# Kernel tuning notes

Measured on AMD Instinct MI355X. Metric: run time of the kernel, lower is better.

## Reference

```python
import jax, jax.numpy as jnp
import numpy as np

MAX_RADIUS = 1.5
NUM_BASIS = 10
CS, CV = 16, 4              # scalar / vector multiplicities (input = query = key = output irreps)
DIM = CS + 3 * CV           # 28
SILU_GAIN = 1.679           # e3nn normalize2mom gain for silu


def _sus(x):
    # e3nn soft_unit_step: exp(-1/x) for x>0 else 0
    xp = jnp.where(x > 0, x, 1.0)
    return jnp.where(x > 0, jnp.exp(-1.0 / xp), 0.0)


def _fc(emb, w1, w2):
    # FullyConnectedNet([NUM_BASIS, 16, numel], act=silu), fan-in normalized
    h = SILU_GAIN * jax.nn.silu(emb @ w1 / jnp.sqrt(float(NUM_BASIS)))
    return h @ w2 / jnp.sqrt(16.0)


def _tp(fs, fv, sh1, w):
    # FullyConnectedTensorProduct((CS x0e + CV x1o) x (1x0e + 1x1o)) with per-edge weights w [...,400]
    # paths: 0e*0e->0e, 0e*1o->1o, 1o*0e->1o, 1o*1o->0e (sh l=0 component == 1)
    i0 = CS * CS; i1 = i0 + CS * CV; i2 = i1 + CV * CV
    lead = w.shape[:-1]
    w1 = w[..., :i0].reshape(lead + (CS, CS))
    w2 = w[..., i0:i1].reshape(lead + (CS, CV))
    w3 = w[..., i1:i2].reshape(lead + (CV, CV))
    w4 = w[..., i2:].reshape(lead + (CV, CS))
    out_s = (jnp.einsum('...c,...co->...o', fs, w1) / jnp.sqrt(float(CS))
             + jnp.einsum('...cx,...x,...co->...o', fv, sh1, w4) / jnp.sqrt(3.0 * CV)) / jnp.sqrt(2.0)
    out_v = (jnp.einsum('...c,...x,...co->...ox', fs, sh1, w2) / jnp.sqrt(float(CS))
             + jnp.einsum('...cx,...co->...ox', fv, w3) / jnp.sqrt(float(CV))) / jnp.sqrt(2.0)
    return out_s, out_v


def _forward(f, pos, wq_s, wq_v, fck_w1, fck_w2, fcv_w1, fcv_w2, dot_ws, dot_wv):
    B, N, _ = f.shape
    fs = f[..., :CS]                                    # [B,N,CS]
    fv = f[..., CS:].reshape(B, N, CV, 3)               # [B,N,CV,3]
    valid = jnp.any(f != 0, axis=-1)                    # mask of non-padded nodes

    # dense radius graph: i = dst, j = src; edge_vec = pos[src] - pos[dst]
    dvec = pos[:, None, :, :] - pos[:, :, None, :]      # [B,i,j,3]
    dist = jnp.sqrt(jnp.sum(dvec * dvec, axis=-1) + 1e-12)
    eye = jnp.eye(N, dtype=bool)
    mask = (dist < MAX_RADIUS) & (~eye)[None] & valid[:, :, None] & valid[:, None, :]
    sh1 = jnp.sqrt(3.0) * dvec / dist[..., None]        # component-normalized l=1 spherical harmonics

    # soft_one_hot_linspace, basis='smooth_finite', cutoff=True, scaled by sqrt(NB)
    step = MAX_RADIUS / (NUM_BASIS + 1)
    centers = jnp.linspace(0.0, MAX_RADIUS, NUM_BASIS + 2)[1:-1]
    diff = (dist[..., None] - centers) / step
    emb = (1.14136 * np.e ** 2) * _sus(diff + 1.0) * _sus(1.0 - diff)
    emb = emb * jnp.sqrt(float(NUM_BASIS))
    cutoff = _sus(10.0 * (1.0 - dist / MAX_RADIUS)) * mask

    # q = h_q(f): per-l linear
    q_s = fs @ wq_s / jnp.sqrt(float(CS))
    q_v = jnp.einsum('bncx,co->bnox', fv, wq_v) / jnp.sqrt(float(CV))

    wk = _fc(emb, fck_w1, fck_w2)                       # [B,N,N,400] per-edge TP weights
    wv = _fc(emb, fcv_w1, fcv_w2)
    k_s, k_v = _tp(fs[:, None], fv[:, None], sh1, wk)   # gather f[src] via broadcast over dst axis
    v_s, v_v = _tp(fs[:, None], fv[:, None], sh1, wv)

    # dot(q[dst], k) -> scalar per edge
    score = (jnp.einsum('bic,bijd,cd->bij', q_s, k_s, dot_ws) / jnp.sqrt(float(CS))
             + jnp.einsum('bicx,bijdx,cd->bij', q_v, k_v, dot_wv) / jnp.sqrt(3.0 * CV)) / jnp.sqrt(2.0)
    log_exp = cutoff * score
    z = jnp.sum(log_exp, axis=-1)                       # scatter-sum over src per dst node
    z = jnp.where(z == 0, 1.0, z)
    alpha = log_exp / z[:, :, None]
    r = jax.nn.relu(alpha)
    att = jnp.where(r > 0, jnp.sqrt(jnp.where(r > 0, r, 1.0)), 0.0)

    out_s = jnp.einsum('bij,bijo->bio', att, v_s)       # scatter-aggregate
    out_v = jnp.einsum('bij,bijox->biox', att, v_v)
    out = jnp.concatenate([out_s, out_v.reshape(B, N, 3 * CV)], axis=-1)
    return out * valid[..., None].astype(out.dtype)


def setup_inputs() -> dict:
    key = jax.random.key(0)
    ks = jax.random.split(key, 10)
    B, N = 4, 192
    NUMEL = CS * CS + CS * CV + CV * CV + CV * CS       # 400
    n = jax.random.normal
    return {
        'f': n(ks[0], (B, N, DIM), dtype=jnp.float32),
        'pos': 5.0 * jax.random.uniform(ks[1], (B, N, 3), dtype=jnp.float32),
        'wq_s': n(ks[2], (CS, CS), dtype=jnp.float32),
        'wq_v': n(ks[3], (CV, CV), dtype=jnp.float32),
        'fck_w1': n(ks[4], (NUM_BASIS, 16), dtype=jnp.float32),
        'fck_w2': n(ks[5], (16, NUMEL), dtype=jnp.float32),
        'fcv_w1': n(ks[6], (NUM_BASIS, 16), dtype=jnp.float32),
        'fcv_w2': n(ks[7], (16, NUMEL), dtype=jnp.float32),
        'dot_ws': n(ks[8], (CS, CS), dtype=jnp.float32),
        'dot_wv': n(ks[9], (CV, CV), dtype=jnp.float32),
    }


def reference(f, pos, wq_s, wq_v, fck_w1, fck_w2, fcv_w1, fcv_w2, dot_ws, dot_wv):
    return _forward(f, pos, wq_s, wq_v, fck_w1, fck_w2, fcv_w1, fcv_w2, dot_ws, dot_wv)
```

## Files before the change

### kernel.cpp

```cpp
#include <hip/hip_runtime.h>
#include <math.h>


#define NN 192
#define TSTRIDE 2560
#define MAXM 192
#define NPB 3

constexpr float C1   = 0.17677669529663687f;
constexpr float C2   = 0.17677669529663687f;
constexpr float C3   = 0.35355339059327373f;
constexpr float C4   = 0.20412414523193154f;
constexpr float CS1f = 0.17677669529663687f;
constexpr float CS2f = 0.20412414523193154f;
constexpr float RS10 = 0.31622776601683794f;
constexpr float GAIN4 = 1.679f * 0.25f;
constexpr float SQRT3 = 1.7320508075688772f;
constexpr float CEMB = (float)(1.14136 * 7.3890560989306495 * 3.1622776601683795);

__global__ __launch_bounds__(256) void precomp(
  const float* __restrict__ f, const float* __restrict__ wq_s, const float* __restrict__ wq_v,
  const float* __restrict__ w2k, const float* __restrict__ w2v,
  const float* __restrict__ dws, const float* __restrict__ dwv,
  float* __restrict__ T, float* __restrict__ qd, float* __restrict__ validf, int BN)
{
  const int node0 = blockIdx.x * NPB;
  const int tid   = threadIdx.x;
  __shared__ float Wsh[12800];
  __shared__ float fsh[NPB][28];
  __shared__ float qs_sh[NPB][16], qv_sh[NPB][12];
  __shared__ int vsh[NPB];
  if (tid < NPB) vsh[tid] = 0;
  if (tid < NPB*28) {
    const int n = tid / 28, c = tid - n*28;
    fsh[n][c] = (node0 + n < BN) ? f[(node0 + n)*28 + c] : 0.f;
  }
  {
    float4* d = (float4*)Wsh;
    const float4* s0 = (const float4*)w2k;
    const float4* s1 = (const float4*)w2v;
    for (int q = tid; q < 1600; q += 256) { d[q] = s0[q]; d[1600 + q] = s1[q]; }
  }
  __syncthreads();
  if (tid < NPB*28) {
    const int n = tid / 28, c = tid - n*28;
    if (fsh[n][c] != 0.f) vsh[n] = 1;
    if (c < 16) {
      float a = 0.f;
      #pragma unroll
      for (int c2 = 0; c2 < 16; ++c2) a = fmaf(fsh[n][c2], wq_s[c2*16 + c], a);
      qs_sh[n][c] = a * 0.25f;
    } else {
      const int idx = c - 16, o = idx / 3, x = idx - o*3;
      float a = 0.f;
      #pragma unroll
      for (int c2 = 0; c2 < 4; ++c2) a = fmaf(fsh[n][16 + c2*3 + x], wq_v[c2*4 + o], a);
      qv_sh[n][idx] = a * 0.5f;
    }
  }
  __syncthreads();
  if (tid < NPB*28) {
    const int n = tid / 28, c = tid - n*28, node = node0 + n;
    if (node < BN) {
      if (c < 16) {
        float a = 0.f;
        #pragma unroll
        for (int c2 = 0; c2 < 16; ++c2) a = fmaf(qs_sh[n][c2], dws[c2*16 + c], a);
        qd[node*28 + c] = a * CS1f;
      } else {
        const int idx = c - 16, d2 = idx / 3, x = idx - d2*3;
        float a = 0.f;
        #pragma unroll
        for (int c2 = 0; c2 < 4; ++c2) a = fmaf(qv_sh[n][c2*3 + x], dwv[c2*4 + d2], a);
        qd[node*28 + c] = a * CS2f;
      }
      if (c == 0) validf[node] = vsh[n] ? 1.f : 0.f;
    }
  }

  for (int e = tid; e < NPB*2560; e += 256) {
    const int n = e / 2560;
    if (node0 + n >= BN) break;
    const int rr = e - n*2560;
    const int fc = rr >= 1280 ? 1 : 0;
    const int r = rr - fc*1280;
    const int h = r / 80, q = r - h*80;
    const float* W = Wsh + fc*6400 + h*400;
    const float* fn = fsh[n];
    float val = 0.f;
    if (q < 16) {
      #pragma unroll
      for (int c = 0; c < 16; ++c) val = fmaf(fn[c], W[c*16 + q], val);
      val *= C1;
    } else if (q < 20) {
      const int o = q - 16;
      #pragma unroll
      for (int c = 0; c < 16; ++c) val = fmaf(fn[c], W[256 + c*4 + o], val);
      val *= C2;
    } else if (q < 32) {
      const int p = q - 20, o = p / 3, x = p - o*3;
      #pragma unroll
      for (int c = 0; c < 4; ++c) val = fmaf(fn[16 + c*3 + x], W[320 + c*4 + o], val);
      val *= C3;
    } else {
      const int p = q - 32, o = p / 3, x = p - o*3;
      #pragma unroll
      for (int c = 0; c < 4; ++c) val = fmaf(fn[16 + c*3 + x], W[336 + c*16 + o], val);
      val *= C4;
    }
    T[(size_t)(node0 + n)*TSTRIDE + fc*1280 + (q >> 2)*64 + h*4 + (q & 3)] = val;
  }
}

__global__ __launch_bounds__(256) void se3_main(
  const float* __restrict__ pos, const float* __restrict__ w1k, const float* __restrict__ w1v,
  const float* __restrict__ T, const float* __restrict__ qd, const float* __restrict__ validf,
  float* __restrict__ out)
{
  const int bi = blockIdx.x;
  const int b = bi / NN, i = bi - b*NN;
  const int tid = threadIdx.x;
  const int lane = tid & 63, wid = tid >> 6;

  __shared__ float qd_sh[28];
  __shared__ float w1_sh[320];
  __shared__ int   s_node[MAXM];
  __shared__ float s_cut[MAXM], s_dist[MAXM];
  __shared__ float s_shx[MAXM], s_shy[MAXM], s_shz[MAXM];
  __shared__ float emb_sh[MAXM*10];
  __shared__ float Hk_sh[MAXM*16];
  __shared__ float Hv_sh[MAXM*16];
  __shared__ float le_sh[MAXM];
  __shared__ float att_sh[MAXM];
  __shared__ int   cnt_sh;
  __shared__ float red_sh[4];
  __shared__ float opart[4][28];

  if (tid < 28) qd_sh[tid] = qd[bi*28 + tid];
  if (tid < 160) {
    w1_sh[tid]       = w1k[tid] * RS10;
    w1_sh[160 + tid] = w1v[tid] * RS10;
  }
  if (tid == 0) cnt_sh = 0;
  const float pix = pos[bi*3+0], piy = pos[bi*3+1], piz = pos[bi*3+2];
  const float vali = validf[bi];
  __syncthreads();

  if (tid < NN) {
    const int nj = b*NN + tid;
    const float dx = pos[nj*3+0]-pix, dy = pos[nj*3+1]-piy, dz = pos[nj*3+2]-piz;
    const float dist = sqrtf(fmaf(dx,dx,fmaf(dy,dy,dz*dz)) + 1e-12f);
    if (tid != i && dist < 1.5f && vali != 0.f && validf[nj] != 0.f) {
      const float cut = expf(-1.f / (10.f * (1.f - dist * (1.f/1.5f))));
      if (cut > 0.f) {
        const int s = atomicAdd(&cnt_sh, 1);
        const float sc = SQRT3 / dist;
        s_node[s] = nj; s_cut[s] = cut; s_dist[s] = dist;
        s_shx[s] = dx*sc; s_shy[s] = dy*sc; s_shz[s] = dz*sc;
      }
    }
  }
  __syncthreads();
  const int M = cnt_sh;
  const int MK = M * 16;

  for (int idx = tid; idx < M*10; idx += 256) {
    const int pr = idx / 10, k = idx - pr*10;
    const float dd = (s_dist[pr] - (float)(k+1)*(1.5f/11.f)) * (11.f/1.5f);
    float e = 0.f;
    if (dd > -1.f && dd < 1.f) e = CEMB * expf(-1.f/(1.f+dd) - 1.f/(1.f-dd));
    emb_sh[idx] = e;
  }
  __syncthreads();

  for (int idx = tid; idx < M*32; idx += 256) {
    const int pr = idx >> 5, t = idx & 31, h = t & 15;
    const float* w = w1_sh + (t >> 4)*160;
    const float* e = emb_sh + pr*10;
    float s = 0.f;
    #pragma unroll
    for (int q = 0; q < 10; ++q) s = fmaf(e[q], w[q*16 + h], s);
    const float hh = GAIN4 * s / (1.f + expf(-s));
    float* dst = (t < 16) ? Hk_sh : Hv_sh;
    dst[pr*16 + h] = hh;
  }
  __syncthreads();

  for (int idx = tid; idx < MK; idx += 256) {
    const int pr = idx >> 4, h = idx & 15;
    const int node = s_node[pr];
    const float sx = s_shx[pr], sy = s_shy[pr], sz = s_shz[pr];
    const float a = Hk_sh[idx];
    const float4* b4 = (const float4*)(T + (size_t)node*TSTRIDE);
    float cc[80];
    float4* c4 = (float4*)cc;
    #pragma unroll
    for (int q = 0; q < 20; ++q) c4[q] = b4[q*16 + h];
    float s = 0.f;
    #pragma unroll
    for (int o = 0; o < 16; ++o) {
      const float t4 = fmaf(cc[32+3*o], sx, fmaf(cc[33+3*o], sy, cc[34+3*o]*sz));
      s = fmaf(qd_sh[o], cc[o] + t4, s);
    }
    #pragma unroll
    for (int o = 0; o < 4; ++o) {
      const float qvs = fmaf(qd_sh[16+3*o], sx, fmaf(qd_sh[17+3*o], sy, qd_sh[18+3*o]*sz));
      s = fmaf(qvs, cc[16+o], s);
      s = fmaf(qd_sh[16+3*o], cc[20+3*o+0], s);
      s = fmaf(qd_sh[17+3*o], cc[20+3*o+1], s);
      s = fmaf(qd_sh[18+3*o], cc[20+3*o+2], s);
    }
    s *= a;
    #pragma unroll
    for (int d = 1; d < 16; d <<= 1) s += __shfl_xor(s, d);
    if ((tid & 15) == 0) le_sh[pr] = s;
  }
  __syncthreads();

  float les = 0.f;
  if (tid < M) les = s_cut[tid] * le_sh[tid];
  float z = les;
  #pragma unroll
  for (int d = 1; d < 64; d <<= 1) z += __shfl_xor(z, d);
  if (lane == 0) red_sh[wid] = z;
  __syncthreads();
  z = red_sh[0] + red_sh[1] + red_sh[2] + red_sh[3];
  if (z == 0.f) z = 1.f;
  if (tid < M) {
    const float alpha = les / z;
    att_sh[tid] = alpha > 0.f ? sqrtf(alpha) : 0.f;
  }
  __syncthreads();

  float acc[28];
  #pragma unroll
  for (int c = 0; c < 28; ++c) acc[c] = 0.f;
  for (int idx = tid; idx < MK; idx += 256) {
    const int pr = idx >> 4, h = idx & 15;
    const int node = s_node[pr];
    const float sx = s_shx[pr], sy = s_shy[pr], sz = s_shz[pr];
    const float a = Hv_sh[idx] * att_sh[pr];
    const float4* b4 = (const float4*)(T + (size_t)node*TSTRIDE + 1280);
    float cc[80];
    float4* c4 = (float4*)cc;
    #pragma unroll
    for (int q = 0; q < 20; ++q) c4[q] = b4[q*16 + h];
    #pragma unroll
    for (int o = 0; o < 16; ++o) {
      const float t4 = fmaf(cc[32+3*o], sx, fmaf(cc[33+3*o], sy, cc[34+3*o]*sz));
      acc[o] = fmaf(a, cc[o] + t4, acc[o]);
    }
    const float ax = a*sx, ay = a*sy, az = a*sz;
    #pragma unroll
    for (int o = 0; o < 4; ++o) {
      const float t2 = cc[16+o];
      acc[16+3*o+0] = fmaf(ax, t2, fmaf(a, cc[20+3*o+0], acc[16+3*o+0]));
      acc[16+3*o+1] = fmaf(ay, t2, fmaf(a, cc[20+3*o+1], acc[16+3*o+1]));
      acc[16+3*o+2] = fmaf(az, t2, fmaf(a, cc[20+3*o+2], acc[16+3*o+2]));
    }
  }

  #pragma unroll
  for (int c = 0; c < 28; ++c) {
    float w = acc[c];
    #pragma unroll
    for (int d = 1; d < 64; d <<= 1) w += __shfl_xor(w, d);
    if (lane == 0) opart[wid][c] = w;
  }
  __syncthreads();
  if (tid < 28) out[bi*28 + tid] = opart[0][tid] + opart[1][tid] + opart[2][tid] + opart[3][tid];
}

extern "C" void kernel_launch(void* const* d_in, const int* in_sizes, int n_in,
                              void* d_out, int out_size, void* d_ws, size_t ws_size,
                              hipStream_t stream) {
  const float* f      = (const float*)d_in[0];
  const float* pos    = (const float*)d_in[1];
  const float* wq_s   = (const float*)d_in[2];
  const float* wq_v   = (const float*)d_in[3];
  const float* fck_w1 = (const float*)d_in[4];
  const float* fck_w2 = (const float*)d_in[5];
  const float* fcv_w1 = (const float*)d_in[6];
  const float* fcv_w2 = (const float*)d_in[7];
  const float* dot_ws = (const float*)d_in[8];
  const float* dot_wv = (const float*)d_in[9];
  float* outp = (float*)d_out;

  const int BN = in_sizes[0] / 28;

  float* T   = (float*)d_ws;
  float* qdp = T + (size_t)BN * TSTRIDE;
  float* vf  = qdp + (size_t)BN * 28;

  const int pblocks = (BN + NPB - 1) / NPB;
  precomp<<<pblocks, 256, 0, stream>>>(f, wq_s, wq_v, fck_w2, fcv_w2, dot_ws, dot_wv, T, qdp, vf, BN);
  se3_main<<<BN, 256, 0, stream>>>(pos, fck_w1, fcv_w1, T, qdp, vf, outp);
}
```

Baseline: 112.6 us.

## Repartition precompute kernel by weight row and node group

The precompute kernel now gives each block 16 nodes and one of 32 (fc,h) weight rows, loading only a 400-float weight row instead of staging the full 12800-float weight matrix in shared memory for 3 nodes. This removes the large per-block shared-memory fill and the low occupancy it forces. The query/dot and valid-flag work moves to the ch==0 blocks. The kernel drops its bounds checks and assumes BN is a multiple of 16. It also calls __syncthreads inside a branch, which is only safe because ch is uniform across the block.

Measured after the change: 105.0 us. 1.07x faster.

```diff
diff --git a/kernel.cpp b/kernel.cpp
--- a/kernel.cpp
+++ b/kernel.cpp
@@ -5,7 +5,7 @@
 #define NN 192
 #define TSTRIDE 2560
 #define MAXM 192
-#define NPB 3
+#define GN 16
 
 constexpr float C1   = 0.17677669529663687f;
 constexpr float C2   = 0.17677669529663687f;
@@ -18,50 +18,80 @@
 constexpr float SQRT3 = 1.7320508075688772f;
 constexpr float CEMB = (float)(1.14136 * 7.3890560989306495 * 3.1622776601683795);
 
-__global__ __launch_bounds__(256) void precomp(
+__global__ __launch_bounds__(256) void precomp_T(
   const float* __restrict__ f, const float* __restrict__ wq_s, const float* __restrict__ wq_v,
   const float* __restrict__ w2k, const float* __restrict__ w2v,
   const float* __restrict__ dws, const float* __restrict__ dwv,
-  float* __restrict__ T, float* __restrict__ qd, float* __restrict__ validf, int BN)
+  float* __restrict__ T, float* __restrict__ qd, float* __restrict__ validf)
 {
-  const int node0 = blockIdx.x * NPB;
-  const int tid   = threadIdx.x;
-  __shared__ float Wsh[12800];
-  __shared__ float fsh[NPB][28];
-  __shared__ float qs_sh[NPB][16], qv_sh[NPB][12];
-  __shared__ int vsh[NPB];
-  if (tid < NPB) vsh[tid] = 0;
-  if (tid < NPB*28) {
-    const int n = tid / 28, c = tid - n*28;
-    fsh[n][c] = (node0 + n < BN) ? f[(node0 + n)*28 + c] : 0.f;
-  }
+  const int bid = blockIdx.x;
+  const int ng = bid >> 5, ch = bid & 31;
+  const int fc = ch >> 4, h = ch & 15;
+  const int node0 = ng * GN;
+  const int tid = threadIdx.x;
+
+  __shared__ float Wrow[400];
+  __shared__ float fsh[GN][28];
+  __shared__ float qs_sh[GN][16], qv_sh[GN][12];
+  __shared__ int   vsh[GN];
+
   {
-    float4* d = (float4*)Wsh;
-    const float4* s0 = (const float4*)w2k;
-    const float4* s1 = (const float4*)w2v;
-    for (int q = tid; q < 1600; q += 256) { d[q] = s0[q]; d[1600 + q] = s1[q]; }
-  }
-  __syncthreads();
-  if (tid < NPB*28) {
-    const int n = tid / 28, c = tid - n*28;
-    if (fsh[n][c] != 0.f) vsh[n] = 1;
-    if (c < 16) {
-      float a = 0.f;
-      #pragma unroll
-      for (int c2 = 0; c2 < 16; ++c2) a = fmaf(fsh[n][c2], wq_s[c2*16 + c], a);
-      qs_sh[n][c] = a * 0.25f;
+    const float* Wsrc = (fc ? w2v : w2k) + h*400;
+    if (tid < 100) ((float4*)Wrow)[tid] = ((const float4*)Wsrc)[tid];
+    else if (tid < 212) ((float4*)fsh)[tid - 100] = ((const float4*)(f + node0*28))[tid - 100];
+    if (tid < GN) vsh[tid] = 0;
+  }
+  __syncthreads();
+
+  #pragma unroll
+  for (int k = 0; k < 5; ++k) {
+    const int out = tid + k*256;
+    const int n = out / 80, q = out - n*80;
+    const float* fn = fsh[n];
+    float val = 0.f;
+    if (q < 16) {
+      #pragma unroll
+      for (int c = 0; c < 16; ++c) val = fmaf(fn[c], Wrow[c*16 + q], val);
+      val *= C1;
+    } else if (q < 20) {
+      const int o = q - 16;
+      #pragma unroll
+      for (int c = 0; c < 16; ++c) val = fmaf(fn[c], Wrow[256 + c*4 + o], val);
+      val *= C2;
+    } else if (q < 32) {
+      const int p = q - 20, o = p / 3, x = p - o*3;
+      #pragma unroll
+      for (int c = 0; c < 4; ++c) val = fmaf(fn[16 + c*3 + x], Wrow[320 + c*4 + o], val);
+      val *= C3;
     } else {
-      const int idx = c - 16, o = idx / 3, x = idx - o*3;
-      float a = 0.f;
-      #pragma unroll
-      for (int c2 = 0; c2 < 4; ++c2) a = fmaf(fsh[n][16 + c2*3 + x], wq_v[c2*4 + o], a);
-      qv_sh[n][idx] = a * 0.5f;
-    }
-  }
-  __syncthreads();
-  if (tid < NPB*28) {
-    const int n = tid / 28, c = tid - n*28, node = node0 + n;
-    if (node < BN) {
+      const int p = q - 32, o = p / 3, x = p - o*3;
+      #pragma unroll
+      for (int c = 0; c < 4; ++c) val = fmaf(fn[16 + c*3 + x], Wrow[336 + c*16 + o], val);
+      val *= C4;
+    }
+    T[(size_t)(node0 + n)*TSTRIDE + fc*1280 + (q >> 2)*64 + h*4 + (q & 3)] = val;
+  }
+
+  if (ch == 0) {
+    for (int t = tid; t < GN*28; t += 256) {
+      const int n = t / 28, c = t - n*28;
+      if (fsh[n][c] != 0.f) vsh[n] = 1;
+      if (c < 16) {
+        float a = 0.f;
+        #pragma unroll
+        for (int c2 = 0; c2 < 16; ++c2) a = fmaf(fsh[n][c2], wq_s[c2*16 + c], a);
+        qs_sh[n][c] = a * 0.25f;
+      } else {
+        const int idx = c - 16, o = idx / 3, x = idx - o*3;
+        float a = 0.f;
+        #pragma unroll
+        for (int c2 = 0; c2 < 4; ++c2) a = fmaf(fsh[n][16 + c2*3 + x], wq_v[c2*4 + o], a);
+        qv_sh[n][idx] = a * 0.5f;
+      }
+    }
+    __syncthreads();
+    for (int t = tid; t < GN*28; t += 256) {
+      const int n = t / 28, c = t - n*28, node = node0 + n;
       if (c < 16) {
         float a = 0.f;
         #pragma unroll
@@ -76,39 +106,6 @@
       }
       if (c == 0) validf[node] = vsh[n] ? 1.f : 0.f;
     }
-  }
-
-  for (int e = tid; e < NPB*2560; e += 256) {
-    const int n = e / 2560;
-    if (node0 + n >= BN) break;
-    const int rr = e - n*2560;
-    const int fc = rr >= 1280 ? 1 : 0;
-    const int r = rr - fc*1280;
-    const int h = r / 80, q = r - h*80;
-    const float* W = Wsh + fc*6400 + h*400;
-    const float* fn = fsh[n];
-    float val = 0.f;
-    if (q < 16) {
-      #pragma unroll
-      for (int c = 0; c < 16; ++c) val = fmaf(fn[c], W[c*16 + q], val);
-      val *= C1;
-    } else if (q < 20) {
-      const int o = q - 16;
-      #pragma unroll
-      for (int c = 0; c < 16; ++c) val = fmaf(fn[c], W[256 + c*4 + o], val);
-      val *= C2;
-    } else if (q < 32) {
-      const int p = q - 20, o = p / 3, x = p - o*3;
-      #pragma unroll
-      for (int c = 0; c < 4; ++c) val = fmaf(fn[16 + c*3 + x], W[320 + c*4 + o], val);
-      val *= C3;
-    } else {
-      const int p = q - 32, o = p / 3, x = p - o*3;
-      #pragma unroll
-      for (int c = 0; c < 4; ++c) val = fmaf(fn[16 + c*3 + x], W[336 + c*16 + o], val);
-      val *= C4;
-    }
-    T[(size_t)(node0 + n)*TSTRIDE + fc*1280 + (q >> 2)*64 + h*4 + (q & 3)] = val;
   }
 }
 
@@ -292,7 +289,7 @@
   float* qdp = T + (size_t)BN * TSTRIDE;
   float* vf  = qdp + (size_t)BN * 28;
 
-  const int pblocks = (BN + NPB - 1) / NPB;
-  precomp<<<pblocks, 256, 0, stream>>>(f, wq_s, wq_v, fck_w2, fcv_w2, dot_ws, dot_wv, T, qdp, vf, BN);
+  const int NG = (BN + GN - 1) / GN;
+  precomp_T<<<NG * 32, 256, 0, stream>>>(f, wq_s, wq_v, fck_w2, fcv_w2, dot_ws, dot_wv, T, qdp, vf);
   se3_main<<<BN, 256, 0, stream>>>(pos, fck_w1, fcv_w1, T, qdp, vf, outp);
 }
```
